# Kernel optimization log

Measured on AMD Instinct MI355X. Metric: run time of the kernel, lower is better.

The kernel has to match this reference:

```python
import jax, jax.numpy as jnp
import numpy as np

B, S, D, H = 2, 2048, 1024, 16
Dh = D // H

def setup_inputs() -> dict:
    key = jax.random.key(0)
    ks = jax.random.split(key, 11)
    def lin(k, fan_in):
        bound = 1.0 / np.sqrt(fan_in)
        kw, kb = jax.random.split(k)
        W = jax.random.uniform(kw, (D, D), jnp.float32, -bound, bound)
        b = jax.random.uniform(kb, (D,), jnp.float32, -bound, bound)
        return W, b
    Wq, bq = lin(ks[0], D)
    Wk, bk = lin(ks[1], D)
    Wv, bv = lin(ks[2], D)
    Wo, bo = lin(ks[3], D)
    Q = jax.random.normal(ks[4], (B, S, D), jnp.float32)
    K = jax.random.normal(ks[5], (B, S, D), jnp.float32)
    V = jax.random.normal(ks[6], (B, S, D), jnp.float32)
    return {"Q": Q, "K": K, "V": V, "Wq": Wq, "bq": bq, "Wk": Wk, "bk": bk,
            "Wv": Wv, "bv": bv, "Wo": Wo, "bo": bo}

def _split_heads(x):
    # [B,S,D] -> [B,H,S,Dh]
    b, s, _ = x.shape
    return x.reshape(b, s, H, Dh).transpose(0, 2, 1, 3)

def reference(Q, K, V, Wq, bq, Wk, bk, Wv, bv, Wo, bo):
    q = _split_heads(Q @ Wq.T + bq)
    k = _split_heads(K @ Wk.T + bk)
    v = _split_heads(V @ Wv.T + bv)
    scores = jnp.einsum('bhqd,bhkd->bhqk', q, k) / jnp.sqrt(jnp.float32(Dh))
    attn = jax.nn.softmax(scores, axis=-1)
    out = jnp.einsum('bhqk,bhkd->bhqd', attn, v)  # [B,H,S,Dh]
    out = out.transpose(0, 2, 1, 3).reshape(Q.shape[0], Q.shape[1], D)
    return out @ Wo.T + bo
```

## Files before the change

kernel.cpp:

```cpp
#include <hip/hip_runtime.h>

#define SEQ 2048
#define DMODEL 1024
#define NH 16
#define DH 64

typedef __attribute__((ext_vector_type(8))) short bf16x8;
typedef __attribute__((ext_vector_type(4))) short bf16x4;
typedef __attribute__((ext_vector_type(4))) float floatx4;
typedef __attribute__((ext_vector_type(4))) unsigned short u16x4;
typedef unsigned short u16;
typedef unsigned int u32;

typedef const void __attribute__((address_space(1)))* as1cvp;
typedef void __attribute__((address_space(3)))* as3vp;

__device__ __forceinline__ void glds16(const void* g, void* l) {
    __builtin_amdgcn_global_load_lds((as1cvp)g, (as3vp)l, 16, 0, 0);
}

__device__ __forceinline__ u16 f2bf(float f) {
    union { u32 u; float f; } v; v.f = f;
    return (u16)((v.u + 0x8000u) >> 16);
}

__device__ __forceinline__ u32 pk2(float a, float b) {
    union { u32 u; float f; } x, y; x.f = a; y.f = b;
    u32 xr = x.u + 0x8000u, yr = y.u + 0x8000u;
#if __has_builtin(__builtin_amdgcn_perm)
    return __builtin_amdgcn_perm(yr, xr, 0x07060302u);
#else
    return (xr >> 16) | (yr & 0xffff0000u);
#endif
}

__device__ __forceinline__ float ex2(float x) {
#if __has_builtin(__builtin_amdgcn_exp2f)
    return __builtin_amdgcn_exp2f(x);
#else
    float r; asm("v_exp_f32 %0, %1" : "=v"(r) : "v"(x)); return r;
#endif
}

__device__ __forceinline__ floatx4 mfma32(bf16x8 a, bf16x8 b, floatx4 c) {
    return __builtin_amdgcn_mfma_f32_16x16x32_bf16(a, b, c, 0, 0, 0);
}

__device__ __forceinline__ uint4 cvt8(const float* __restrict__ p) {
    float4 a = *(const float4*)p;
    float4 b = *(const float4*)(p + 4);
    uint4 q;
    q.x = pk2(a.x, a.y); q.y = pk2(a.z, a.w);
    q.z = pk2(b.x, b.y); q.w = pk2(b.z, b.w);
    return q;
}

#define QSCALE 0.18033688011112042f

__global__ __launch_bounds__(256) void cvt_all(
    const float* __restrict__ Q, const float* __restrict__ K, const float* __restrict__ V,
    const float* __restrict__ W0, const float* __restrict__ W1,
    const float* __restrict__ W2, const float* __restrict__ W3,
    u16* __restrict__ Qb, u16* __restrict__ Kb, u16* __restrict__ Vb,
    u16* __restrict__ Wb)
{
    const int y = blockIdx.y;
    const float* src; u16* dst;
    if (y == 0)      { src = Q;  dst = Qb; }
    else if (y == 1) { src = K;  dst = Kb; }
    else if (y == 2) { src = V;  dst = Vb; }
    else {
        if (blockIdx.x >= 512) return;
        src = (y == 3) ? W0 : (y == 4) ? W1 : (y == 5) ? W2 : W3;
        dst = Wb + (size_t)(y - 3) * 1048576;
    }
    size_t i = ((size_t)blockIdx.x * 256 + threadIdx.x) * 8;
    *(uint4*)(dst + i) = cvt8(src + i);
}

__global__ __launch_bounds__(256) void cvt_w(
    const float* __restrict__ W0, const float* __restrict__ W1,
    const float* __restrict__ W2, const float* __restrict__ W3,
    u16* __restrict__ out)
{
    const float* src = (blockIdx.y == 0) ? W0 : (blockIdx.y == 1) ? W1
                     : (blockIdx.y == 2) ? W2 : W3;
    size_t i = ((size_t)blockIdx.x * 256 + threadIdx.x) * 8;
    *(uint4*)(out + (size_t)blockIdx.y * 1048576 + i) = cvt8(src + i);
}

__device__ __forceinline__ void qkv_store(
    int z, u16* __restrict__ outp, int rowg, int col, floatx4 a4, float bv, float sc)
{
    union { u32 w[2]; u16 h[4]; u16x4 v4; } pk;
    pk.w[0] = pk2((a4[0] + bv) * sc, (a4[1] + bv) * sc);
    pk.w[1] = pk2((a4[2] + bv) * sc, (a4[3] + bv) * sc);
    int b = rowg >> 11, s = rowg & 2047, h = col >> 6, d = col & 63;
    if (z < 2) {
#pragma unroll
        for (int r = 0; r < 4; r++)
            outp[((size_t)(b * NH + h) * SEQ + s + r) * DH + d] = pk.h[r];
    } else {
        *(u16x4*)(outp + ((size_t)(b * NH + h) * DH + d) * SEQ + s) = pk.v4;
    }
}

__global__ __launch_bounds__(256) void gemm_qkv_bb(
    const u16* __restrict__ Qb, const u16* __restrict__ Kb, const u16* __restrict__ Vb,
    const u16* __restrict__ Wb,
    const float* __restrict__ b0, const float* __restrict__ b1, const float* __restrict__ b2,
    u16* __restrict__ qo, u16* __restrict__ ko, u16* __restrict__ vto)
{
    __shared__ __align__(16) u16 As[3][4096];
    __shared__ __align__(16) u16 Bs[3][4096];
    const int tid = threadIdx.x, l = tid & 63, w = tid >> 6;
    const int lm = l & 15, quad = l >> 4;
    const int wr = (w >> 1) * 64, wc = (w & 1) * 64;
    const int orig = blockIdx.x + 8 * blockIdx.y + 256 * blockIdx.z;
    const int swz  = (orig & 7) * 96 + (orig >> 3);
    const int z    = swz >> 8;
    const int rem  = swz & 255;
    const int bm = (rem >> 3) * 128, bn = (rem & 7) * 128;
    const u16* A      = (z == 0) ? Qb : (z == 1) ? Kb : Vb;
    const u16* W      = Wb + (size_t)z * 1048576;
    const float* bias = (z == 0) ? b0 : (z == 1) ? b1 : b2;

    const int srow = tid >> 2, scol = (tid & 3) * 8;

    floatx4 acc[4][4];
#pragma unroll
    for (int i = 0; i < 4; i++)
#pragma unroll
        for (int j = 0; j < 4; j++) acc[i][j] = (floatx4){0.f, 0.f, 0.f, 0.f};

#define QKV_STAGE(I, NB) do { \
        const int kt_ = (I) * 32; \
        glds16(A + (size_t)(bm + srow) * DMODEL + kt_ + scol, As[NB] + w * 512); \
        glds16(A + (size_t)(bm + 64 + srow) * DMODEL + kt_ + scol, As[NB] + 2048 + w * 512); \
        glds16(W + (size_t)(bn + srow) * DMODEL + kt_ + scol, Bs[NB] + w * 512); \
        glds16(W + (size_t)(bn + 64 + srow) * DMODEL + kt_ + scol, Bs[NB] + 2048 + w * 512); \
    } while (0)

    QKV_STAGE(0, 0);
    QKV_STAGE(1, 1);
    asm volatile("s_waitcnt vmcnt(4)" ::: "memory");
    __builtin_amdgcn_s_barrier();

    int cur = 0, nx = 2;
    for (int i = 0; i < 32; i++) {
        bf16x8 af[4], bfr[4];
#pragma unroll
        for (int mi = 0; mi < 4; mi++)
            af[mi] = *(const bf16x8*)(As[cur] + (wr + mi * 16 + lm) * 32 + quad * 8);
#pragma unroll
        for (int ni = 0; ni < 4; ni++)
            bfr[ni] = *(const bf16x8*)(Bs[cur] + (wc + ni * 16 + lm) * 32 + quad * 8);
#pragma unroll
        for (int mi = 0; mi < 4; mi++)
#pragma unroll
            for (int ni = 0; ni < 4; ni++)
                acc[mi][ni] = __builtin_amdgcn_mfma_f32_16x16x32_bf16(
                    af[mi], bfr[ni], acc[mi][ni], 0, 0, 0);

        if (i + 2 < 32) {
            QKV_STAGE(i + 2, nx);
            asm volatile("s_waitcnt vmcnt(4)" ::: "memory");
            __builtin_amdgcn_s_barrier();
        } else if (i + 1 < 32) {
            asm volatile("s_waitcnt vmcnt(0)" ::: "memory");
            __builtin_amdgcn_s_barrier();
        }
        cur = (cur == 2) ? 0 : cur + 1;
        nx  = (nx == 2) ? 0 : nx + 1;
    }
#undef QKV_STAGE

    const float sc = (z == 0) ? QSCALE : 1.0f;
    u16* outp = (z == 0) ? qo : (z == 1) ? ko : vto;
#pragma unroll
    for (int ni = 0; ni < 4; ni++) {
        int col = bn + wc + ni * 16 + lm;
        float bv = bias[col];
#pragma unroll
        for (int mi = 0; mi < 4; mi++)
            qkv_store(z, outp, bm + wr + mi * 16 + quad * 4, col, acc[mi][ni], bv, sc);
    }
}

template<bool WBF>
__global__ __launch_bounds__(256) void gemm_qkv(
    const float* __restrict__ Qf, const float* __restrict__ Kf, const float* __restrict__ Vf,
    const void* __restrict__ W0, const void* __restrict__ W1, const void* __restrict__ W2,
    const float* __restrict__ b0, const float* __restrict__ b1, const float* __restrict__ b2,
    u16* __restrict__ qo, u16* __restrict__ ko, u16* __restrict__ vto)
{
    __shared__ __align__(16) u16 As[128 * 32];
    __shared__ __align__(16) u16 Bs[128 * 32];
    const int tid = threadIdx.x, l = tid & 63, w = tid >> 6;
    const int lm = l & 15, quad = l >> 4;
    const int wr = (w >> 1) * 64, wc = (w & 1) * 64;
    const int bm = blockIdx.y * 128, bn = blockIdx.x * 128;
    const int z = blockIdx.z;
    const float* A    = (z == 0) ? Qf : (z == 1) ? Kf : Vf;
    const void* Wp    = (z == 0) ? W0 : (z == 1) ? W1 : W2;
    const float* bias = (z == 0) ? b0 : (z == 1) ? b1 : b2;

    floatx4 acc[4][4];
#pragma unroll
    for (int i = 0; i < 4; i++)
#pragma unroll
        for (int j = 0; j < 4; j++) acc[i][j] = (floatx4){0.f, 0.f, 0.f, 0.f};

    for (int kt = 0; kt < DMODEL; kt += 32) {
        __syncthreads();
#pragma unroll
        for (int j = 0; j < 2; j++) {
            int ch = j * 256 + tid, row = ch >> 2, c = ch & 3;
            *(uint4*)(As + ch * 8) = cvt8(A + (size_t)(bm + row) * DMODEL + kt + c * 8);
        }
        if (WBF) {
            const u16* Wc = (const u16*)Wp;
            glds16(Wc + (size_t)(bn + (tid >> 2)) * DMODEL + kt + (tid & 3) * 8, Bs + w * 512);
            glds16(Wc + (size_t)(bn + 64 + (tid >> 2)) * DMODEL + kt + (tid & 3) * 8, Bs + 2048 + w * 512);
        } else {
            const float* Wf = (const float*)Wp;
#pragma unroll
            for (int j = 0; j < 2; j++) {
                int ch = j * 256 + tid, row = ch >> 2, c = ch & 3;
                *(uint4*)(Bs + ch * 8) = cvt8(Wf + (size_t)(bn + row) * DMODEL + kt + c * 8);
            }
        }
        __syncthreads();

        bf16x8 af[4], bfr[4];
#pragma unroll
        for (int mi = 0; mi < 4; mi++)
            af[mi] = *(const bf16x8*)(As + (wr + mi * 16 + lm) * 32 + quad * 8);
#pragma unroll
        for (int ni = 0; ni < 4; ni++)
            bfr[ni] = *(const bf16x8*)(Bs + (wc + ni * 16 + lm) * 32 + quad * 8);
#pragma unroll
        for (int mi = 0; mi < 4; mi++)
#pragma unroll
            for (int ni = 0; ni < 4; ni++)
                acc[mi][ni] = __builtin_amdgcn_mfma_f32_16x16x32_bf16(
                    af[mi], bfr[ni], acc[mi][ni], 0, 0, 0);
    }

    const float sc = (z == 0) ? QSCALE : 1.0f;
    u16* outp = (z == 0) ? qo : (z == 1) ? ko : vto;
#pragma unroll
    for (int ni = 0; ni < 4; ni++) {
        int col = bn + wc + ni * 16 + lm;
        float bv = bias[col];
#pragma unroll
        for (int mi = 0; mi < 4; mi++)
            qkv_store(z, outp, bm + wr + mi * 16 + quad * 4, col, acc[mi][ni], bv, sc);
    }
}

__global__ __launch_bounds__(256) void gemm_o_p(
    const u16* __restrict__ A, const u16* __restrict__ W,
    const float* __restrict__ bias, float* __restrict__ out)
{
    __shared__ __align__(16) u16 As[3][4096];
    __shared__ __align__(16) u16 Bs[3][2048];
    const int tid = threadIdx.x, l = tid & 63, w = tid >> 6;
    const int lm = l & 15, quad = l >> 4;
    const int orig = blockIdx.x + 16 * blockIdx.y;
    const int swz  = (orig & 7) * 64 + (orig >> 3);
    const int bm = (swz >> 4) * 128, bn = (swz & 15) * 64;

    floatx4 acc[2][4];
#pragma unroll
    for (int i = 0; i < 2; i++)
#pragma unroll
        for (int j = 0; j < 4; j++) acc[i][j] = (floatx4){0.f, 0.f, 0.f, 0.f};

#define O_STAGE(I, NB) do { \
        const int kt_ = (I) * 32; \
        glds16(A + (size_t)(bm + (tid >> 2)) * DMODEL + kt_ + (tid & 3) * 8, As[NB] + w * 512); \
        glds16(A + (size_t)(bm + 64 + (tid >> 2)) * DMODEL + kt_ + (tid & 3) * 8, As[NB] + 2048 + w * 512); \
        glds16(W + (size_t)(bn + (tid >> 2)) * DMODEL + kt_ + (tid & 3) * 8, Bs[NB] + w * 512); \
    } while (0)

    O_STAGE(0, 0);
    O_STAGE(1, 1);
    asm volatile("s_waitcnt vmcnt(3)" ::: "memory");
    __builtin_amdgcn_s_barrier();

    int cur = 0, nx = 2;
    for (int i = 0; i < 32; i++) {
        bf16x8 af[2], bfr[4];
#pragma unroll
        for (int mi = 0; mi < 2; mi++)
            af[mi] = *(const bf16x8*)(As[cur] + (w * 32 + mi * 16 + lm) * 32 + quad * 8);
#pragma unroll
        for (int ni = 0; ni < 4; ni++)
            bfr[ni] = *(const bf16x8*)(Bs[cur] + (ni * 16 + lm) * 32 + quad * 8);
#pragma unroll
        for (int mi = 0; mi < 2; mi++)
#pragma unroll
            for (int ni = 0; ni < 4; ni++)
                acc[mi][ni] = __builtin_amdgcn_mfma_f32_16x16x32_bf16(
                    af[mi], bfr[ni], acc[mi][ni], 0, 0, 0);

        if (i + 2 < 32) {
            O_STAGE(i + 2, nx);
            asm volatile("s_waitcnt vmcnt(3)" ::: "memory");
            __builtin_amdgcn_s_barrier();
        } else if (i + 1 < 32) {
            asm volatile("s_waitcnt vmcnt(0)" ::: "memory");
            __builtin_amdgcn_s_barrier();
        }
        cur = (cur == 2) ? 0 : cur + 1;
        nx  = (nx == 2) ? 0 : nx + 1;
    }
#undef O_STAGE

#pragma unroll
    for (int ni = 0; ni < 4; ni++) {
        int col = bn + ni * 16 + lm;
        float bv = bias[col];
#pragma unroll
        for (int mi = 0; mi < 2; mi++) {
#pragma unroll
            for (int r = 0; r < 4; r++) {
                int rowg = bm + w * 32 + mi * 16 + quad * 4 + r;
                out[(size_t)rowg * DMODEL + col] = acc[mi][ni][r] + bv;
            }
        }
    }
}

template<bool WBF>
__global__ __launch_bounds__(256) void gemm_o(
    const u16* __restrict__ A, const void* __restrict__ Wp,
    const float* __restrict__ bias, float* __restrict__ out)
{
    __shared__ __align__(16) u16 As[128 * 32];
    __shared__ __align__(16) u16 Bs[64 * 32];
    const int tid = threadIdx.x, l = tid & 63, w = tid >> 6;
    const int lm = l & 15, quad = l >> 4;
    const int bm = blockIdx.y * 128, bn = blockIdx.x * 64;

    floatx4 acc[2][4];
#pragma unroll
    for (int i = 0; i < 2; i++)
#pragma unroll
        for (int j = 0; j < 4; j++) acc[i][j] = (floatx4){0.f, 0.f, 0.f, 0.f};

    for (int kt = 0; kt < DMODEL; kt += 32) {
        __syncthreads();
        glds16(A + (size_t)(bm + (tid >> 2)) * DMODEL + kt + (tid & 3) * 8, As + w * 512);
        glds16(A + (size_t)(bm + 64 + (tid >> 2)) * DMODEL + kt + (tid & 3) * 8, As + 2048 + w * 512);
        if (WBF) {
            glds16((const u16*)Wp + (size_t)(bn + (tid >> 2)) * DMODEL + kt + (tid & 3) * 8, Bs + w * 512);
        } else {
            *(uint4*)(Bs + tid * 8) =
                cvt8((const float*)Wp + (size_t)(bn + (tid >> 2)) * DMODEL + kt + (tid & 3) * 8);
        }
        __syncthreads();

        bf16x8 af[2], bfr[4];
#pragma unroll
        for (int mi = 0; mi < 2; mi++)
            af[mi] = *(const bf16x8*)(As + (w * 32 + mi * 16 + lm) * 32 + quad * 8);
#pragma unroll
        for (int ni = 0; ni < 4; ni++)
            bfr[ni] = *(const bf16x8*)(Bs + (ni * 16 + lm) * 32 + quad * 8);
#pragma unroll
        for (int mi = 0; mi < 2; mi++)
#pragma unroll
            for (int ni = 0; ni < 4; ni++)
                acc[mi][ni] = __builtin_amdgcn_mfma_f32_16x16x32_bf16(
                    af[mi], bfr[ni], acc[mi][ni], 0, 0, 0);
    }

#pragma unroll
    for (int ni = 0; ni < 4; ni++) {
        int col = bn + ni * 16 + lm;
        float bv = bias[col];
#pragma unroll
        for (int mi = 0; mi < 2; mi++) {
#pragma unroll
            for (int r = 0; r < 4; r++) {
                int rowg = bm + w * 32 + mi * 16 + quad * 4 + r;
                out[(size_t)rowg * DMODEL + col] = acc[mi][ni][r] + bv;
            }
        }
    }
}

#define SP 72
#define TS (64 * SP)
#define BUFSZ (4 * TS)
__global__ __launch_bounds__(256, 2) void attn_kernel(
    const u16* __restrict__ q, const u16* __restrict__ k,
    const u16* __restrict__ vt, u16* __restrict__ out)
{
    __shared__ __align__(16) u16 smem[2 * BUFSZ];
    const int tid = threadIdx.x, l = tid & 63, w = tid >> 6;
    const int lm = l & 15, quad = l >> 4;
    const int orig = blockIdx.x + 16 * blockIdx.y;
    const int swz  = (orig & 7) * 64 + (orig >> 3);
    const int qt = swz & 15, bh = swz >> 4;
    const int b = bh >> 4, h = bh & 15;
    const int rg = w & 1, half = w >> 1;

    bf16x8 qf[4][2];
#pragma unroll
    for (int nt = 0; nt < 4; nt++) {
        int row = qt * 128 + rg * 64 + nt * 16 + lm;
        const u16* qp = q + ((size_t)bh * SEQ + row) * DH;
        qf[nt][0] = *(const bf16x8*)(qp + quad * 8);
        qf[nt][1] = *(const bf16x8*)(qp + 32 + quad * 8);
    }

    floatx4 O[4][4];
#pragma unroll
    for (int dt = 0; dt < 4; dt++)
#pragma unroll
        for (int nt = 0; nt < 4; nt++) O[dt][nt] = (floatx4){0.f, 0.f, 0.f, 0.f};
    floatx4 Ol[4];
#pragma unroll
    for (int nt = 0; nt < 4; nt++) Ol[nt] = (floatx4){0.f, 0.f, 0.f, 0.f};

    const bf16x8 ones8 = {(short)0x3F80, (short)0x3F80, (short)0x3F80, (short)0x3F80,
                          (short)0x3F80, (short)0x3F80, (short)0x3F80, (short)0x3F80};

    const int srow = tid >> 2, sc4 = tid & 3;
    const int prow = (srow & 32) | ((srow & 4) << 2) | ((srow & 24) >> 1) | (srow & 3);
    const u16* kbase = k + (size_t)bh * SEQ * DH;
    const u16* vbase = vt + (size_t)bh * DH * SEQ;

    uint4 kA0, kA1, kB0, kB1, vA0, vA1, vB0, vB1;
#define LOADT(T) do { \
        const u16* kgA = kbase + (size_t)((T) * 64 + srow) * DH + sc4 * 16; \
        const u16* kgB = kbase + (size_t)(1024 + (T) * 64 + srow) * DH + sc4 * 16; \
        kA0 = *(const uint4*)kgA;       kA1 = *(const uint4*)(kgA + 8); \
        kB0 = *(const uint4*)kgB;       kB1 = *(const uint4*)(kgB + 8); \
        const u16* vgA = vbase + (size_t)srow * SEQ + (T) * 64 + sc4 * 16; \
        const u16* vgB = vgA + 1024; \
        vA0 = *(const uint4*)vgA;       vA1 = *(const uint4*)(vgA + 8); \
        vB0 = *(const uint4*)vgB;       vB1 = *(const uint4*)(vgB + 8); \
    } while (0)
#define WRBUF(BUF) do { \
        u16* K0 = smem + (BUF) * BUFSZ; \
        u16* K1 = K0 + TS; \
        u16* V0 = K0 + 2 * TS; \
        u16* V1 = K0 + 3 * TS; \
        *(uint4*)(K0 + prow * SP + sc4 * 16)     = kA0; \
        *(uint4*)(K0 + prow * SP + sc4 * 16 + 8) = kA1; \
        *(uint4*)(K1 + prow * SP + sc4 * 16)     = kB0; \
        *(uint4*)(K1 + prow * SP + sc4 * 16 + 8) = kB1; \
        *(uint4*)(V0 + srow * SP + sc4 * 16)     = vA0; \
        *(uint4*)(V0 + srow * SP + sc4 * 16 + 8) = vA1; \
        *(uint4*)(V1 + srow * SP + sc4 * 16)     = vB0; \
        *(uint4*)(V1 + srow * SP + sc4 * 16 + 8) = vB1; \
    } while (0)

    LOADT(0);
    WRBUF(0);
    LOADT(1);
    asm volatile("s_waitcnt lgkmcnt(0)" ::: "memory");
    __builtin_amdgcn_s_barrier();

    for (int t = 0; t < 16; t++) {
        const int cur = t & 1;
        const u16* Kh = smem + cur * BUFSZ + half * TS;
        const u16* Vh = smem + cur * BUFSZ + (2 + half) * TS;

        floatx4 Sc[4][4];
        __builtin_amdgcn_s_setprio(1);
#pragma unroll
        for (int sub = 0; sub < 4; sub++) {
            bf16x8 ka0 = *(const bf16x8*)(Kh + (sub * 16 + lm) * SP + quad * 8);
            bf16x8 ka1 = *(const bf16x8*)(Kh + (sub * 16 + lm) * SP + 32 + quad * 8);
#pragma unroll
            for (int nt = 0; nt < 4; nt++) {
                floatx4 c = (floatx4){0.f, 0.f, 0.f, 0.f};
                c = mfma32(ka0, qf[nt][0], c);
                c = mfma32(ka1, qf[nt][1], c);
                Sc[sub][nt] = c;
            }
        }
        __builtin_amdgcn_s_setprio(0);

        if (t + 1 < 16) {
            asm volatile("s_waitcnt vmcnt(0)" ::: "memory");
            WRBUF(cur ^ 1);
            if (t + 2 < 16) LOADT(t + 2);
        }

        bf16x8 pbm[2][4];
#pragma unroll
        for (int p = 0; p < 2; p++)
#pragma unroll
            for (int nt = 0; nt < 4; nt++) {
                floatx4 sa = Sc[p * 2][nt], sb = Sc[p * 2 + 1][nt];
#pragma unroll
                for (int r = 0; r < 4; r++) { sa[r] = ex2(sa[r]); sb[r] = ex2(sb[r]); }
                union { u32 w4[4]; bf16x8 v; } pku;
                pku.w4[0] = pk2(sa[0], sa[1]);
                pku.w4[1] = pk2(sa[2], sa[3]);
                pku.w4[2] = pk2(sb[0], sb[1]);
                pku.w4[3] = pk2(sb[2], sb[3]);
                pbm[p][nt] = pku.v;
            }

        __builtin_amdgcn_s_setprio(1);
#pragma unroll
        for (int nt = 0; nt < 4; nt++) {
            Ol[nt] = mfma32(ones8, pbm[0][nt], Ol[nt]);
            Ol[nt] = mfma32(ones8, pbm[1][nt], Ol[nt]);
        }

#pragma unroll
        for (int dt = 0; dt < 4; dt++) {
            bf16x8 va0 = *(const bf16x8*)(Vh + (dt * 16 + lm) * SP + quad * 8);
            bf16x8 va1 = *(const bf16x8*)(Vh + (dt * 16 + lm) * SP + 32 + quad * 8);
#pragma unroll
            for (int nt = 0; nt < 4; nt++) {
                O[dt][nt] = mfma32(va0, pbm[0][nt], O[dt][nt]);
                O[dt][nt] = mfma32(va1, pbm[1][nt], O[dt][nt]);
            }
        }
        __builtin_amdgcn_s_setprio(0);

        asm volatile("s_waitcnt lgkmcnt(0)" ::: "memory");
        __builtin_amdgcn_s_barrier();
    }
#undef LOADT
#undef WRBUF

    float* obuf  = (float*)smem;
    float* mlbuf = (float*)smem + 8704;
    if (w >= 2) {
        float* ob = obuf + (rg * 64 + l) * 68;
        float* ml = mlbuf + (rg * 64 + l) * 5;
#pragma unroll
        for (int nt = 0; nt < 4; nt++) {
#pragma unroll
            for (int dt = 0; dt < 4; dt++)
                *(floatx4*)(ob + nt * 16 + dt * 4) = O[dt][nt];
            ml[nt] = Ol[nt][0];
        }
    }
    __syncthreads();
    if (w < 2) {
        float* ob = obuf + (rg * 64 + l) * 68;
        float* ml = mlbuf + (rg * 64 + l) * 5;
#pragma unroll
        for (int nt = 0; nt < 4; nt++) {
            float lB = ml[nt];
            float inv = 1.0f / (Ol[nt][0] + lB);
            int s = qt * 128 + rg * 64 + nt * 16 + lm;
            u16* op = out + ((size_t)b * SEQ + s) * DMODEL + h * DH;
#pragma unroll
            for (int dt = 0; dt < 4; dt++) {
                floatx4 Ob = *(const floatx4*)(ob + nt * 16 + dt * 4);
                union { u32 w2[2]; u16x4 v; } pku;
                pku.w2[0] = pk2((O[dt][nt][0] + Ob[0]) * inv,
                                (O[dt][nt][1] + Ob[1]) * inv);
                pku.w2[1] = pk2((O[dt][nt][2] + Ob[2]) * inv,
                                (O[dt][nt][3] + Ob[3]) * inv);
                *(u16x4*)(op + dt * 16 + quad * 4) = pku.v;
            }
        }
    }
}

extern "C" void kernel_launch(void* const* d_in, const int* in_sizes, int n_in,
                              void* d_out, int out_size, void* d_ws, size_t ws_size,
                              hipStream_t stream) {
    (void)in_sizes; (void)n_in; (void)out_size;
    const float* Q  = (const float*)d_in[0];
    const float* K  = (const float*)d_in[1];
    const float* V  = (const float*)d_in[2];
    const float* Wq = (const float*)d_in[3];
    const float* bq = (const float*)d_in[4];
    const float* Wk = (const float*)d_in[5];
    const float* bk = (const float*)d_in[6];
    const float* Wv = (const float*)d_in[7];
    const float* bv = (const float*)d_in[8];
    const float* Wo = (const float*)d_in[9];
    const float* bo = (const float*)d_in[10];

    const size_t NEL = (size_t)2 * NH * SEQ * DH;
    u16* base = (u16*)d_ws;
    dim3 bb(256);
    dim3 ab(256);

    if (ws_size >= 8 * NEL * 2) {
        u16* Qb   = base;
        u16* Kb   = Qb + NEL;
        u16* Vb   = Kb + NEL;
        u16* Wb   = Vb + NEL;
        u16* qws  = Wb + NEL;
        u16* kws  = qws + NEL;
        u16* vtws = kws + NEL;
        u16* aws  = vtws + NEL;
        cvt_all<<<dim3(2048, 7), bb, 0, stream>>>(Q, K, V, Wq, Wk, Wv, Wo, Qb, Kb, Vb, Wb);
        gemm_qkv_bb<<<dim3(8, 32, 3), bb, 0, stream>>>(
            Qb, Kb, Vb, Wb, bq, bk, bv, qws, kws, vtws);
        attn_kernel<<<dim3(SEQ / 128, 2 * NH), ab, 0, stream>>>(qws, kws, vtws, aws);
        gemm_o_p<<<dim3(16, 32), bb, 0, stream>>>(aws, Wb + 3145728, bo, (float*)d_out);
    } else if (ws_size >= 5 * NEL * 2) {
        u16* Wb = base;
        u16* qws = base + NEL; u16* kws = qws + NEL; u16* vtws = kws + NEL; u16* aws = vtws + NEL;
        cvt_w<<<dim3(512, 4), bb, 0, stream>>>(Wq, Wk, Wv, Wo, Wb);
        gemm_qkv<true><<<dim3(8, 32, 3), bb, 0, stream>>>(
            Q, K, V, Wb, Wb + 1048576, Wb + 2097152, bq, bk, bv, qws, kws, vtws);
        attn_kernel<<<dim3(SEQ / 128, 2 * NH), ab, 0, stream>>>(qws, kws, vtws, aws);
        gemm_o_p<<<dim3(16, 32), bb, 0, stream>>>(aws, Wb + 3145728, bo, (float*)d_out);
    } else {
        u16* qws = base; u16* kws = qws + NEL; u16* vtws = kws + NEL; u16* aws = vtws + NEL;
        gemm_qkv<false><<<dim3(8, 32, 3), bb, 0, stream>>>(
            Q, K, V, Wq, Wk, Wv, bq, bk, bv, qws, kws, vtws);
        attn_kernel<<<dim3(SEQ / 128, 2 * NH), ab, 0, stream>>>(qws, kws, vtws, aws);
        gemm_o<false><<<dim3(16, 32), bb, 0, stream>>>(aws, Wo, bo, (float*)d_out);
    }
}
```

Measured before the change: 209.1 us.

## Double attention block to 512 threads with 32 query rows per wave

The attention kernel now launches 512 threads (8 waves) per block instead of 256. Each wave handles 32 query rows instead of 64, with the two key halves still split across wave groups. K/V tile loads are spread over twice as many threads, and each wave's score computation, exp and packing is interleaved per pair of key subtiles before the next tile's LDS write is issued. The aim is more waves per CU to hide latency and fewer registers per wave, at the cost of reloading K/V fragments from LDS per wave, i.e. more LDS read traffic per query row.

New measurement: 206.8 us (median of 2 runs). No clear change (-1.1%).

```diff
diff --git a/kernel.cpp b/kernel.cpp
--- a/kernel.cpp
+++ b/kernel.cpp
@@ -395,7 +395,7 @@
 #define SP 72
 #define TS (64 * SP)
 #define BUFSZ (4 * TS)
-__global__ __launch_bounds__(256, 2) void attn_kernel(
+__global__ __launch_bounds__(512, 2) void attn_kernel(
     const u16* __restrict__ q, const u16* __restrict__ k,
     const u16* __restrict__ vt, u16* __restrict__ out)
 {
@@ -406,58 +406,48 @@
     const int swz  = (orig & 7) * 64 + (orig >> 3);
     const int qt = swz & 15, bh = swz >> 4;
     const int b = bh >> 4, h = bh & 15;
-    const int rg = w & 1, half = w >> 1;
-
-    bf16x8 qf[4][2];
-#pragma unroll
-    for (int nt = 0; nt < 4; nt++) {
-        int row = qt * 128 + rg * 64 + nt * 16 + lm;
+    const int rg = w & 3, half = w >> 2;
+
+    bf16x8 qf[2][2];
+#pragma unroll
+    for (int nt = 0; nt < 2; nt++) {
+        int row = qt * 128 + rg * 32 + nt * 16 + lm;
         const u16* qp = q + ((size_t)bh * SEQ + row) * DH;
         qf[nt][0] = *(const bf16x8*)(qp + quad * 8);
         qf[nt][1] = *(const bf16x8*)(qp + 32 + quad * 8);
     }
 
-    floatx4 O[4][4];
+    floatx4 O[4][2];
 #pragma unroll
     for (int dt = 0; dt < 4; dt++)
 #pragma unroll
-        for (int nt = 0; nt < 4; nt++) O[dt][nt] = (floatx4){0.f, 0.f, 0.f, 0.f};
-    floatx4 Ol[4];
-#pragma unroll
-    for (int nt = 0; nt < 4; nt++) Ol[nt] = (floatx4){0.f, 0.f, 0.f, 0.f};
+        for (int nt = 0; nt < 2; nt++) O[dt][nt] = (floatx4){0.f, 0.f, 0.f, 0.f};
+    floatx4 Ol[2] = {(floatx4){0.f,0.f,0.f,0.f}, (floatx4){0.f,0.f,0.f,0.f}};
 
     const bf16x8 ones8 = {(short)0x3F80, (short)0x3F80, (short)0x3F80, (short)0x3F80,
                           (short)0x3F80, (short)0x3F80, (short)0x3F80, (short)0x3F80};
 
-    const int srow = tid >> 2, sc4 = tid & 3;
+    const int srow = tid >> 3, sc = tid & 7;
     const int prow = (srow & 32) | ((srow & 4) << 2) | ((srow & 24) >> 1) | (srow & 3);
     const u16* kbase = k + (size_t)bh * SEQ * DH;
     const u16* vbase = vt + (size_t)bh * DH * SEQ;
 
-    uint4 kA0, kA1, kB0, kB1, vA0, vA1, vB0, vB1;
+    uint4 kA, kB, vA, vB;
 #define LOADT(T) do { \
-        const u16* kgA = kbase + (size_t)((T) * 64 + srow) * DH + sc4 * 16; \
-        const u16* kgB = kbase + (size_t)(1024 + (T) * 64 + srow) * DH + sc4 * 16; \
-        kA0 = *(const uint4*)kgA;       kA1 = *(const uint4*)(kgA + 8); \
-        kB0 = *(const uint4*)kgB;       kB1 = *(const uint4*)(kgB + 8); \
-        const u16* vgA = vbase + (size_t)srow * SEQ + (T) * 64 + sc4 * 16; \
-        const u16* vgB = vgA + 1024; \
-        vA0 = *(const uint4*)vgA;       vA1 = *(const uint4*)(vgA + 8); \
-        vB0 = *(const uint4*)vgB;       vB1 = *(const uint4*)(vgB + 8); \
+        kA = *(const uint4*)(kbase + (size_t)((T) * 64 + srow) * DH + sc * 8); \
+        kB = *(const uint4*)(kbase + (size_t)(1024 + (T) * 64 + srow) * DH + sc * 8); \
+        vA = *(const uint4*)(vbase + (size_t)srow * SEQ + (T) * 64 + sc * 8); \
+        vB = *(const uint4*)(vbase + (size_t)srow * SEQ + 1024 + (T) * 64 + sc * 8); \
     } while (0)
 #define WRBUF(BUF) do { \
         u16* K0 = smem + (BUF) * BUFSZ; \
         u16* K1 = K0 + TS; \
         u16* V0 = K0 + 2 * TS; \
         u16* V1 = K0 + 3 * TS; \
-        *(uint4*)(K0 + prow * SP + sc4 * 16)     = kA0; \
-        *(uint4*)(K0 + prow * SP + sc4 * 16 + 8) = kA1; \
-        *(uint4*)(K1 + prow * SP + sc4 * 16)     = kB0; \
-        *(uint4*)(K1 + prow * SP + sc4 * 16 + 8) = kB1; \
-        *(uint4*)(V0 + srow * SP + sc4 * 16)     = vA0; \
-        *(uint4*)(V0 + srow * SP + sc4 * 16 + 8) = vA1; \
-        *(uint4*)(V1 + srow * SP + sc4 * 16)     = vB0; \
-        *(uint4*)(V1 + srow * SP + sc4 * 16 + 8) = vB1; \
+        *(uint4*)(K0 + prow * SP + sc * 8) = kA; \
+        *(uint4*)(K1 + prow * SP + sc * 8) = kB; \
+        *(uint4*)(V0 + srow * SP + sc * 8) = vA; \
+        *(uint4*)(V1 + srow * SP + sc * 8) = vB; \
     } while (0)
 
     LOADT(0);
@@ -471,34 +461,28 @@
         const u16* Kh = smem + cur * BUFSZ + half * TS;
         const u16* Vh = smem + cur * BUFSZ + (2 + half) * TS;
 
-        floatx4 Sc[4][4];
-        __builtin_amdgcn_s_setprio(1);
-#pragma unroll
-        for (int sub = 0; sub < 4; sub++) {
-            bf16x8 ka0 = *(const bf16x8*)(Kh + (sub * 16 + lm) * SP + quad * 8);
-            bf16x8 ka1 = *(const bf16x8*)(Kh + (sub * 16 + lm) * SP + 32 + quad * 8);
-#pragma unroll
-            for (int nt = 0; nt < 4; nt++) {
-                floatx4 c = (floatx4){0.f, 0.f, 0.f, 0.f};
-                c = mfma32(ka0, qf[nt][0], c);
-                c = mfma32(ka1, qf[nt][1], c);
-                Sc[sub][nt] = c;
+        bf16x8 pbm[2][2];
+#pragma unroll
+        for (int p = 0; p < 2; p++) {
+            floatx4 Sc0[2], Sc1[2];
+            __builtin_amdgcn_s_setprio(1);
+#pragma unroll
+            for (int s = 0; s < 2; s++) {
+                const int sub = p * 2 + s;
+                bf16x8 ka0 = *(const bf16x8*)(Kh + (sub * 16 + lm) * SP + quad * 8);
+                bf16x8 ka1 = *(const bf16x8*)(Kh + (sub * 16 + lm) * SP + 32 + quad * 8);
+#pragma unroll
+                for (int nt = 0; nt < 2; nt++) {
+                    floatx4 c = (floatx4){0.f, 0.f, 0.f, 0.f};
+                    c = mfma32(ka0, qf[nt][0], c);
+                    c = mfma32(ka1, qf[nt][1], c);
+                    if (s == 0) Sc0[nt] = c; else Sc1[nt] = c;
+                }
             }
-        }
-        __builtin_amdgcn_s_setprio(0);
-
-        if (t + 1 < 16) {
-            asm volatile("s_waitcnt vmcnt(0)" ::: "memory");
-            WRBUF(cur ^ 1);
-            if (t + 2 < 16) LOADT(t + 2);
-        }
-
-        bf16x8 pbm[2][4];
-#pragma unroll
-        for (int p = 0; p < 2; p++)
-#pragma unroll
-            for (int nt = 0; nt < 4; nt++) {
-                floatx4 sa = Sc[p * 2][nt], sb = Sc[p * 2 + 1][nt];
+            __builtin_amdgcn_s_setprio(0);
+#pragma unroll
+            for (int nt = 0; nt < 2; nt++) {
+                floatx4 sa = Sc0[nt], sb = Sc1[nt];
 #pragma unroll
                 for (int r = 0; r < 4; r++) { sa[r] = ex2(sa[r]); sb[r] = ex2(sb[r]); }
                 union { u32 w4[4]; bf16x8 v; } pku;
@@ -508,10 +492,17 @@
                 pku.w4[3] = pk2(sb[2], sb[3]);
                 pbm[p][nt] = pku.v;
             }
+        }
+
+        if (t + 1 < 16) {
+            asm volatile("s_waitcnt vmcnt(0)" ::: "memory");
+            WRBUF(cur ^ 1);
+            if (t + 2 < 16) LOADT(t + 2);
+        }
 
         __builtin_amdgcn_s_setprio(1);
 #pragma unroll
-        for (int nt = 0; nt < 4; nt++) {
+        for (int nt = 0; nt < 2; nt++) {
             Ol[nt] = mfma32(ones8, pbm[0][nt], Ol[nt]);
             Ol[nt] = mfma32(ones8, pbm[1][nt], Ol[nt]);
         }
@@ -521,7 +512,7 @@
             bf16x8 va0 = *(const bf16x8*)(Vh + (dt * 16 + lm) * SP + quad * 8);
             bf16x8 va1 = *(const bf16x8*)(Vh + (dt * 16 + lm) * SP + 32 + quad * 8);
 #pragma unroll
-            for (int nt = 0; nt < 4; nt++) {
+            for (int nt = 0; nt < 2; nt++) {
                 O[dt][nt] = mfma32(va0, pbm[0][nt], O[dt][nt]);
                 O[dt][nt] = mfma32(va1, pbm[1][nt], O[dt][nt]);
             }
@@ -535,12 +526,12 @@
 #undef WRBUF
 
     float* obuf  = (float*)smem;
-    float* mlbuf = (float*)smem + 8704;
-    if (w >= 2) {
-        float* ob = obuf + (rg * 64 + l) * 68;
-        float* ml = mlbuf + (rg * 64 + l) * 5;
-#pragma unroll
-        for (int nt = 0; nt < 4; nt++) {
+    float* mlbuf = (float*)smem + 9216;
+    if (half == 1) {
+        float* ob = obuf + (rg * 64 + l) * 36;
+        float* ml = mlbuf + (rg * 64 + l) * 2;
+#pragma unroll
+        for (int nt = 0; nt < 2; nt++) {
 #pragma unroll
             for (int dt = 0; dt < 4; dt++)
                 *(floatx4*)(ob + nt * 16 + dt * 4) = O[dt][nt];
@@ -548,14 +539,14 @@
         }
     }
     __syncthreads();
-    if (w < 2) {
-        float* ob = obuf + (rg * 64 + l) * 68;
-        float* ml = mlbuf + (rg * 64 + l) * 5;
-#pragma unroll
-        for (int nt = 0; nt < 4; nt++) {
+    if (half == 0) {
+        float* ob = obuf + (rg * 64 + l) * 36;
+        float* ml = mlbuf + (rg * 64 + l) * 2;
+#pragma unroll
+        for (int nt = 0; nt < 2; nt++) {
             float lB = ml[nt];
             float inv = 1.0f / (Ol[nt][0] + lB);
-            int s = qt * 128 + rg * 64 + nt * 16 + lm;
+            int s = qt * 128 + rg * 32 + nt * 16 + lm;
             u16* op = out + ((size_t)b * SEQ + s) * DMODEL + h * DH;
 #pragma unroll
             for (int dt = 0; dt < 4; dt++) {
@@ -590,7 +581,7 @@
     const size_t NEL = (size_t)2 * NH * SEQ * DH;
     u16* base = (u16*)d_ws;
     dim3 bb(256);
-    dim3 ab(256);
+    dim3 ab(512);
 
     if (ws_size >= 8 * NEL * 2) {
         u16* Qb   = base;
```
